# Performance work log

Hardware: AMD Instinct MI355X
Metric: run time of the kernel (lower is better)

Reference implementation:

```python
import jax, jax.numpy as jnp
import numpy as np
import math

B, S, H, NH = 4, 1024, 1024, 16
DH = H // NH
G = 100  # native graph size


def setup_inputs() -> dict:
    key = jax.random.key(0)
    ks = jax.random.split(key, 12)
    sc = 1.0 / math.sqrt(H)
    return {
        "v": jax.random.normal(ks[0], (B, S, H), jnp.float32),
        "k": jax.random.normal(ks[1], (B, S, H), jnp.float32),
        "q": jax.random.normal(ks[2], (B, S, H), jnp.float32),
        "mask": jax.random.randint(ks[3], (B, 1, 1, S), 0, 2) == 1,
        "graph": jax.random.uniform(ks[4], (B, G, G), jnp.float32),
        "Wq": jax.random.normal(ks[5], (H, H), jnp.float32) * sc,
        "bq": jnp.zeros((H,), jnp.float32),
        "Wk": jax.random.normal(ks[6], (H, H), jnp.float32) * sc,
        "bk": jnp.zeros((H,), jnp.float32),
        "Wv": jax.random.normal(ks[7], (H, H), jnp.float32) * sc,
        "bv": jnp.zeros((H,), jnp.float32),
        "Wm": jax.random.normal(ks[8], (H, H), jnp.float32) * sc,
        "bm": jnp.zeros((H,), jnp.float32),
    }


def _heads(x, W, b):
    # [B,S,H] -> [B,NH,S,DH]
    y = x @ W + b
    return y.reshape(B, S, NH, DH).transpose(0, 2, 1, 3)


def reference(v, k, q, mask, graph, Wq, bq, Wk, bk, Wv, bv, Wm, bm):
    qh = _heads(q, Wq, bq)
    kh = _heads(k, Wk, bk)
    vh = _heads(v, Wv, bv)
    scores = jnp.einsum("bhqd,bhkd->bhqk", qh, kh) / math.sqrt(DH)
    # pad 100x100 graph to SxS (zeros outside top-left block), as in torch source
    if S > G:
        graph = jnp.zeros((B, S, S), graph.dtype).at[:, :G, :G].set(graph)
    # scores - scores*graph, then mask fill and softmax
    scores = scores - scores * graph[:, None, :, :]
    scores = jnp.where(mask, jnp.float32(-1e9), scores)
    att = jax.nn.softmax(scores, axis=-1)  # dropout is identity in eval
    out = jnp.einsum("bhqk,bhkd->bhqd", att, vh)
    out = out.transpose(0, 2, 1, 3).reshape(B, S, H)
    return out @ Wm + bm
```

## Files before the change

kernel.cpp:

```cpp
#include <hip/hip_runtime.h>
#include <hip/hip_bf16.h>
#include <cstdio>

#define S_ 1024
#define H_ 1024
#define NH_ 16
#define DH_ 64
#define G_ 100

typedef __attribute__((ext_vector_type(8))) short bf16x8;
typedef __attribute__((ext_vector_type(4))) short bf16x4;
typedef __attribute__((ext_vector_type(4))) float f32x4;

__device__ __forceinline__ f32x4 mfma16(bf16x8 a, bf16x8 b, f32x4 c) {
  return __builtin_amdgcn_mfma_f32_16x16x32_bf16(a, b, c, 0, 0, 0);
}

__device__ __forceinline__ short f2bf(float f) {
  union { float f; unsigned int i; } x;
  x.f = f;
  unsigned int r = x.i + 0x7fff + ((x.i >> 16) & 1);
  return (short)(r >> 16);
}

__device__ __forceinline__ unsigned cvtpk(float lo, float hi) {
  unsigned r;
  asm("v_cvt_pk_bf16_f32 %0, %1, %2" : "=v"(r) : "v"(lo), "v"(hi));
  return r;
}

__device__ __forceinline__ float exp2hw(float x) {
  float r;
  asm("v_exp_f32 %0, %1" : "=v"(r) : "v"(x));
  return r;
}

__device__ __forceinline__ void gload16(const void* g, void* l) {
  __builtin_amdgcn_global_load_lds(
      (const __attribute__((address_space(1))) unsigned int*)g,
      (__attribute__((address_space(3))) unsigned int*)l, 16, 0, 0);
}

__global__ __launch_bounds__(256) void transpose_w(
    const float* __restrict__ W0, const float* __restrict__ W1,
    const float* __restrict__ W2, const float* __restrict__ W3,
    short* __restrict__ T0, short* __restrict__ T1,
    short* __restrict__ T2, short* __restrict__ T3) {
  __shared__ short tile[64][72];
  const float* W = (blockIdx.z == 0) ? W0 : (blockIdx.z == 1) ? W1
                 : (blockIdx.z == 2) ? W2 : W3;
  short* T = (blockIdx.z == 0) ? T0 : (blockIdx.z == 1) ? T1
           : (blockIdx.z == 2) ? T2 : T3;
  const int t = threadIdx.x;
  const int r0 = t >> 3;
  const int c8 = (t & 7) * 8;
  const int kbase = blockIdx.x * 64, nbase = blockIdx.y * 64;
#pragma unroll
  for (int p = 0; p < 2; ++p) {
    int r = p * 32 + r0;
    const float* src = W + (size_t)(kbase + r) * H_ + nbase + c8;
    f32x4 u0 = *reinterpret_cast<const f32x4*>(src);
    f32x4 u1 = *reinterpret_cast<const f32x4*>(src + 4);
#pragma unroll
    for (int j = 0; j < 4; ++j) {
      tile[r][c8 + j] = f2bf(u0[j]);
      tile[r][c8 + 4 + j] = f2bf(u1[j]);
    }
  }
  __syncthreads();
#pragma unroll
  for (int p = 0; p < 2; ++p) {
    int r = p * 32 + r0;
    bf16x8 o;
#pragma unroll
    for (int j = 0; j < 8; ++j) o[j] = tile[c8 + j][r];
    *reinterpret_cast<bf16x8*>(T + (size_t)(nbase + r) * H_ + kbase + c8) = o;
  }
}

__global__ __launch_bounds__(256, 3) void qkv128f(
    const float* __restrict__ A0, const float* __restrict__ A1,
    const float* __restrict__ A2, const short* __restrict__ W0,
    const short* __restrict__ W1, const short* __restrict__ W2,
    const float* __restrict__ b0, const float* __restrict__ b1,
    const float* __restrict__ b2, short* __restrict__ O0,
    short* __restrict__ O1, short* __restrict__ O2) {
  __shared__ float Af[2][128 * 32];
  __shared__ short Bs[2][128 * 32];
  const int z = blockIdx.z;
  const float* A  = (z == 0) ? A0 : (z == 1) ? A1 : A2;
  const short* Bt = (z == 0) ? W0 : (z == 1) ? W1 : W2;
  const float* bias = (z == 0) ? b0 : (z == 1) ? b1 : b2;
  short* Cb = (z == 0) ? O0 : (z == 1) ? O1 : O2;
  const float scale = (z == 0) ? 0.18033688f : 1.0f;
  const int K = H_;
  const int t = threadIdx.x;
  const int l = t & 63, w = t >> 6;
  const int lr = l & 15, lg = l >> 4;
  const int lx = lr & 7;
  const int lk = (lr >> 1) & 3;
  const int wm = w >> 1, wn = w & 1;
  const int bm = blockIdx.x * 128, bn = blockIdx.y * 128;
  f32x4 acc[4][4];
#pragma unroll
  for (int i = 0; i < 4; ++i)
#pragma unroll
    for (int j = 0; j < 4; ++j) acc[i][j] = (f32x4){0.f, 0.f, 0.f, 0.f};

  const int ar = t >> 3;
  const float* Ab = A + (size_t)(bm + ar) * K + ((t & 7) ^ (ar & 7)) * 4;
  const int br = t >> 2;
  const short* Bb =
      Bt + (size_t)(bn + br) * K + ((t & 3) ^ ((br >> 1) & 3)) * 8;

  auto stage = [&](int buf, int kb) {
#pragma unroll
    for (int p = 0; p < 4; ++p)
      gload16(Ab + (size_t)p * 32 * K + kb,
              (char*)&Af[buf][0] + p * 4096 + t * 16);
#pragma unroll
    for (int p = 0; p < 2; ++p)
      gload16(Bb + (size_t)p * 64 * K + kb,
              (char*)&Bs[buf][0] + p * 4096 + t * 16);
  };

  stage(0, 0);
  __syncthreads();
  const int NT = K >> 5;
  for (int tt = 0; tt < NT; ++tt) {
    const int cur = tt & 1;
    bf16x8 af[4], bfr[4];
#pragma unroll
    for (int mi = 0; mi < 4; ++mi) {
      const int row = wm * 64 + mi * 16 + lr;
      const float* Ar = &Af[cur][row * 32];
      f32x4 alo = *reinterpret_cast<const f32x4*>(Ar + (((lg * 2) ^ lx) * 4));
      f32x4 ahi =
          *reinterpret_cast<const f32x4*>(Ar + (((lg * 2 + 1) ^ lx) * 4));
      union { unsigned u[4]; bf16x8 v; } c;
      c.u[0] = cvtpk(alo[0], alo[1]);
      c.u[1] = cvtpk(alo[2], alo[3]);
      c.u[2] = cvtpk(ahi[0], ahi[1]);
      c.u[3] = cvtpk(ahi[2], ahi[3]);
      af[mi] = c.v;
    }
#pragma unroll
    for (int ni = 0; ni < 4; ++ni) {
      const int rb = wn * 64 + ni * 16 + lr;
      bfr[ni] = *reinterpret_cast<const bf16x8*>(
          &Bs[cur][rb * 32 + ((lg ^ lk) * 8)]);
    }
    if (tt + 1 < NT) stage(cur ^ 1, (tt + 1) << 5);
#pragma unroll
    for (int mi = 0; mi < 4; ++mi)
#pragma unroll
      for (int ni = 0; ni < 4; ++ni)
        acc[mi][ni] = mfma16(af[mi], bfr[ni], acc[mi][ni]);
    __syncthreads();
  }
#pragma unroll
  for (int mi = 0; mi < 4; ++mi)
#pragma unroll
    for (int ni = 0; ni < 4; ++ni) {
      int col = bn + wn * 64 + ni * 16 + lr;
      float bv = bias[col];
      int h = col >> 6, d = col & 63;
      if (z == 2) {
        int row0 = bm + wm * 64 + mi * 16 + lg * 4;
        int b = row0 >> 10, s0 = row0 & 1023;
        bf16x4 pk;
#pragma unroll
        for (int r = 0; r < 4; ++r) pk[r] = f2bf(acc[mi][ni][r] + bv);
        *reinterpret_cast<bf16x4*>(
            Cb + (((size_t)(b * NH_ + h)) * DH_ + d) * S_ + s0) = pk;
      } else {
#pragma unroll
        for (int r = 0; r < 4; ++r) {
          int row = bm + wm * 64 + mi * 16 + lg * 4 + r;
          int b = row >> 10, s = row & 1023;
          Cb[(((size_t)(b * NH_ + h)) * S_ + s) * DH_ + d] =
              f2bf((acc[mi][ni][r] + bv) * scale);
        }
      }
    }
}

__global__ __launch_bounds__(256) void out64(
    const short* __restrict__ A, const short* __restrict__ Bt,
    const float* __restrict__ bias, float* __restrict__ Cf) {
  __shared__ short As[2][64 * 32];
  __shared__ short Bs[2][128 * 32];
  const int K = H_, N = H_;
  const int t = threadIdx.x;
  const int l = t & 63, w = t >> 6;
  const int lr = l & 15, lg = l >> 4;
  const int lk = (lr >> 1) & 3;
  const int wm = w >> 1, wn = w & 1;
  const int bm = blockIdx.x * 64, bn = blockIdx.y * 128;
  f32x4 acc[2][4];
#pragma unroll
  for (int i = 0; i < 2; ++i)
#pragma unroll
    for (int j = 0; j < 4; ++j) acc[i][j] = (f32x4){0.f, 0.f, 0.f, 0.f};
  const int sr = t >> 2;
  const int ss = ((t & 3) ^ ((sr >> 1) & 3)) * 8;
  const short* Ab = A + (size_t)(bm + sr) * K + ss;
  const short* Bb = Bt + (size_t)(bn + sr) * K + ss;

  auto stage = [&](int buf, int kb) {
    gload16(Ab + kb, (char*)&As[buf][0] + t * 16);
    gload16(Bb + kb, (char*)&Bs[buf][0] + t * 16);
    gload16(Bb + (size_t)64 * K + kb, (char*)&Bs[buf][0] + 4096 + t * 16);
  };

  stage(0, 0);
  __syncthreads();
  const int NT = K >> 5;
  for (int tt = 0; tt < NT; ++tt) {
    const int cur = tt & 1;
    bf16x8 af[2], bfr[4];
#pragma unroll
    for (int mi = 0; mi < 2; ++mi) {
      const int row = wm * 32 + mi * 16 + lr;
      af[mi] = *reinterpret_cast<const bf16x8*>(
          &As[cur][row * 32 + ((lg ^ lk) * 8)]);
    }
#pragma unroll
    for (int ni = 0; ni < 4; ++ni) {
      const int rb = wn * 64 + ni * 16 + lr;
      bfr[ni] = *reinterpret_cast<const bf16x8*>(
          &Bs[cur][rb * 32 + ((lg ^ lk) * 8)]);
    }
    if (tt + 1 < NT) stage(cur ^ 1, (tt + 1) << 5);
#pragma unroll
    for (int mi = 0; mi < 2; ++mi)
#pragma unroll
      for (int ni = 0; ni < 4; ++ni)
        acc[mi][ni] = mfma16(af[mi], bfr[ni], acc[mi][ni]);
    __syncthreads();
  }
#pragma unroll
  for (int mi = 0; mi < 2; ++mi)
#pragma unroll
    for (int ni = 0; ni < 4; ++ni) {
      int col = bn + wn * 64 + ni * 16 + lr;
      float bv = bias[col];
#pragma unroll
      for (int r = 0; r < 4; ++r) {
        int row = bm + wm * 32 + mi * 16 + lg * 4 + r;
        Cf[(size_t)row * N + col] = acc[mi][ni][r] + bv;
      }
    }
}

__global__ __launch_bounds__(256) void attn(
    const short* __restrict__ Qh, const short* __restrict__ Kh,
    const short* __restrict__ VhT, const float* __restrict__ graph,
    const int* __restrict__ mask, short* __restrict__ ctx) {
  __shared__ short Kb[64 * 64];
  __shared__ short Vb[64 * 64];
  __shared__ short P[4 * 16 * 64];
  __shared__ float maskf[S_];
  const int lin = blockIdx.x;
  const int gid = (lin & 7) * 128 + (lin >> 3);
  const int bh = gid >> 4, qt = gid & 15;
  const int b = bh >> 4, h = bh & 15;
  const int t = threadIdx.x, w = t >> 6, l = t & 63;
  const int lr = l & 15, lg = l >> 4;
  const int lx = lr & 7;
  const int q0 = qt * 64 + w * 16;
  const int qg = q0 + lr;
  short* Pw = P + w * 1024;
  const short* Qrow = Qh + ((size_t)bh * S_ + qg) * DH_;
  bf16x8 qf0 = *reinterpret_cast<const bf16x8*>(Qrow + lg * 8);
  bf16x8 qf1 = *reinterpret_cast<const bf16x8*>(Qrow + 32 + lg * 8);
  f32x4 o[4];
#pragma unroll
  for (int i = 0; i < 4; ++i) o[i] = (f32x4){0.f, 0.f, 0.f, 0.f};
  float llp = 0.f;

  const int rs = t >> 2;
  const int ga = (t & 3) + ((rs & 1) << 2);
  const int gb = ga ^ 4;
  const int sw0 = ((ga ^ (rs & 7)) * 8);
  const int sw1 = ((gb ^ (rs & 7)) * 8);
  const short* Ksrc0 = Kh + ((size_t)bh * S_ + rs) * DH_ + ga * 8;
  const short* Ksrc1 = Kh + ((size_t)bh * S_ + rs) * DH_ + gb * 8;
  const short* Vsrc0 = VhT + ((size_t)bh * DH_ + rs) * S_ + ga * 8;
  const short* Vsrc1 = VhT + ((size_t)bh * DH_ + rs) * S_ + gb * 8;

  {
    int4 mv = reinterpret_cast<const int4*>(mask + b * S_)[t];
    f32x4 mo;
    const float C = -16.0f;
    mo.x = mv.x ? -1.0e9f : C;
    mo.y = mv.y ? -1.0e9f : C;
    mo.z = mv.z ? -1.0e9f : C;
    mo.w = mv.w ? -1.0e9f : C;
    reinterpret_cast<f32x4*>(maskf)[t] = mo;
  }
  {
    int4 ka = *reinterpret_cast<const int4*>(Ksrc0);
    int4 kb2 = *reinterpret_cast<const int4*>(Ksrc1);
    int4 va = *reinterpret_cast<const int4*>(Vsrc0);
    int4 vb2 = *reinterpret_cast<const int4*>(Vsrc1);
    *reinterpret_cast<int4*>(&Kb[rs * 64 + sw0]) = ka;
    *reinterpret_cast<int4*>(&Kb[rs * 64 + sw1]) = kb2;
    *reinterpret_cast<int4*>(&Vb[rs * 64 + sw0]) = va;
    *reinterpret_cast<int4*>(&Vb[rs * 64 + sw1]) = vb2;
  }
  __syncthreads();

  for (int kc = 0; kc < S_; kc += 64) {
    const bool pf = (kc + 64 < S_);
    int4 ka, kb2, va, vb2;
    if (pf) {
      ka = *reinterpret_cast<const int4*>(Ksrc0 + (size_t)(kc + 64) * DH_);
      kb2 = *reinterpret_cast<const int4*>(Ksrc1 + (size_t)(kc + 64) * DH_);
      va = *reinterpret_cast<const int4*>(Vsrc0 + kc + 64);
      vb2 = *reinterpret_cast<const int4*>(Vsrc1 + kc + 64);
    }
    f32x4 sacc[4];
    __builtin_amdgcn_s_setprio(1);
#pragma unroll
    for (int mf = 0; mf < 4; ++mf) {
      const int rk = mf * 16 + lr;
      bf16x8 k0 = *reinterpret_cast<const bf16x8*>(
          &Kb[rk * 64 + ((lg ^ lx) * 8)]);
      bf16x8 k1 = *reinterpret_cast<const bf16x8*>(
          &Kb[rk * 64 + (((4 + lg) ^ lx) * 8)]);
      f32x4 sa = (f32x4){0.f, 0.f, 0.f, 0.f};
      sa = mfma16(k0, qf0, sa);
      sa = mfma16(k1, qf1, sa);
      sacc[mf] = sa;
    }
    __builtin_amdgcn_s_setprio(0);
    const bool gblk = (q0 < G_) && (kc < G_);
    const int pw0 = lr * 64 + (lg & 1) * 4;
#pragma unroll
    for (int mf = 0; mf < 4; ++mf) {
      f32x4 mk = *reinterpret_cast<const f32x4*>(&maskf[kc + mf * 16 + lg * 4]);
      f32x4 sa = sacc[mf];
      if (gblk) {
#pragma unroll
        for (int r = 0; r < 4; ++r) {
          int kg = kc + mf * 16 + lg * 4 + r;
          if (qg < G_ && kg < G_)
            sa[r] *= (1.f - graph[((size_t)b * G_ + qg) * G_ + kg]);
        }
      }
      float e0 = exp2hw(sa[0] + mk[0]);
      float e1 = exp2hw(sa[1] + mk[1]);
      float e2 = exp2hw(sa[2] + mk[2]);
      float e3 = exp2hw(sa[3] + mk[3]);
      llp += (e0 + e1) + (e2 + e3);
      int2 pk2;
      pk2.x = (int)cvtpk(e0, e1);
      pk2.y = (int)cvtpk(e2, e3);
      *reinterpret_cast<int2*>(
          &Pw[pw0 + (((2 * mf + (lg >> 1)) ^ lx) * 8)]) = pk2;
    }
    __builtin_amdgcn_s_setprio(1);
#pragma unroll
    for (int ks = 0; ks < 2; ++ks) {
      bf16x8 pa = *reinterpret_cast<const bf16x8*>(
          &Pw[lr * 64 + (((ks * 4 + lg) ^ lx) * 8)]);
#pragma unroll
      for (int nf = 0; nf < 4; ++nf) {
        const int rv = nf * 16 + lr;
        bf16x8 vfr = *reinterpret_cast<const bf16x8*>(
            &Vb[rv * 64 + (((ks * 4 + lg) ^ lx) * 8)]);
        o[nf] = mfma16(pa, vfr, o[nf]);
      }
    }
    __builtin_amdgcn_s_setprio(0);
    if (pf) {
      __syncthreads();
      *reinterpret_cast<int4*>(&Kb[rs * 64 + sw0]) = ka;
      *reinterpret_cast<int4*>(&Kb[rs * 64 + sw1]) = kb2;
      *reinterpret_cast<int4*>(&Vb[rs * 64 + sw0]) = va;
      *reinterpret_cast<int4*>(&Vb[rs * 64 + sw1]) = vb2;
      __syncthreads();
    }
  }
  llp += __shfl_xor(llp, 16);
  llp += __shfl_xor(llp, 32);
  float rinv[4];
#pragma unroll
  for (int r = 0; r < 4; ++r)
    rinv[r] = __builtin_amdgcn_rcpf(__shfl(llp, lg * 4 + r, 64));
#pragma unroll
  for (int nf = 0; nf < 4; ++nf)
#pragma unroll
    for (int r = 0; r < 4; ++r) {
      float val = o[nf][r] * rinv[r];
      ctx[((size_t)b * S_ + q0 + lg * 4 + r) * H_ + h * DH_ + nf * 16 + lr] =
          f2bf(val);
    }
}

extern "C" void kernel_launch(void* const* d_in, const int* in_sizes, int n_in,
                              void* d_out, int out_size, void* d_ws, size_t ws_size,
                              hipStream_t stream) {
  const int B = in_sizes[0] / (S_ * H_);
  const int M = B * S_;
  const float* v    = (const float*)d_in[0];
  const float* k    = (const float*)d_in[1];
  const float* q    = (const float*)d_in[2];
  const int*   mask = (const int*)d_in[3];
  const float* graph= (const float*)d_in[4];
  const float* Wq   = (const float*)d_in[5];
  const float* bq   = (const float*)d_in[6];
  const float* Wk   = (const float*)d_in[7];
  const float* bk   = (const float*)d_in[8];
  const float* Wv   = (const float*)d_in[9];
  const float* bv   = (const float*)d_in[10];
  const float* Wm   = (const float*)d_in[11];
  const float* bm   = (const float*)d_in[12];

  short* ws = (short*)d_ws;
  const size_t WSZ = (size_t)H_ * H_;
  const size_t TSZ = (size_t)M * H_;
  short* WqT = ws;
  short* WkT = ws + WSZ;
  short* WvT = ws + 2 * WSZ;
  short* WmT = ws + 3 * WSZ;
  short* Qh  = ws + 4 * WSZ;
  short* Kh  = Qh + TSZ;
  short* VhT = Kh + TSZ;
  short* ctx = VhT + TSZ;
  if (ws_size < (4 * WSZ + 4 * TSZ) * sizeof(short)) {
    fprintf(stderr, "kernel_launch: ws too small (%zu)\n", ws_size);
    return;
  }

  transpose_w<<<dim3(H_ / 64, H_ / 64, 4), 256, 0, stream>>>(
      Wq, Wk, Wv, Wm, WqT, WkT, WvT, WmT);
  qkv128f<<<dim3(M / 128, H_ / 128, 3), 256, 0, stream>>>(
      q, k, v, WqT, WkT, WvT, bq, bk, bv, Qh, Kh, VhT);
  attn<<<dim3(1024), 256, 0, stream>>>(Qh, Kh, VhT, graph, mask, ctx);
  out64<<<dim3(M / 64, H_ / 128), 256, 0, stream>>>(
      ctx, WmT, bm, (float*)d_out);
}
```

Measured before the change: 106.9 us.

## Compact unmasked key positions and skip masked keys in K/V projection and attention

Adds a per-batch compaction kernel that builds a prefix-sum index list of unmasked key positions and their counts. The K and V projections then compute only rows for gathered unmasked positions, and attention iterates only over the compacted key range, with the graph term remapped through the index list. This is meant to cut projection and attention work roughly in proportion to the masked fraction. The cost is an extra small launch and gathered row loads. Padded tail rows in the last tile are filled with index 0 and hidden by the mask.

New measurement: 101.3 us, median of 2. -5.2%, faster.

```diff
diff --git a/kernel.cpp b/kernel.cpp
--- a/kernel.cpp
+++ b/kernel.cpp
@@ -39,6 +39,47 @@
   __builtin_amdgcn_global_load_lds(
       (const __attribute__((address_space(1))) unsigned int*)g,
       (__attribute__((address_space(3))) unsigned int*)l, 16, 0, 0);
+}
+
+__global__ __launch_bounds__(256) void compact(
+    const int* __restrict__ mask, int* __restrict__ idx,
+    int* __restrict__ cnts) {
+  __shared__ int ps[256];
+  __shared__ int scnt;
+  const int b = blockIdx.x, t = threadIdx.x;
+  int4 mv = reinterpret_cast<const int4*>(mask + b * S_)[t];
+  const int k0 = (mv.x == 0), k1 = (mv.y == 0), k2 = (mv.z == 0),
+            k3 = (mv.w == 0);
+  const int c = k0 + k1 + k2 + k3;
+  ps[t] = c;
+  __syncthreads();
+  for (int off = 1; off < 256; off <<= 1) {
+    int v = (t >= off) ? ps[t - off] : 0;
+    __syncthreads();
+    ps[t] += v;
+    __syncthreads();
+  }
+  int j = ps[t] - c;
+  const int s0 = t * 4;
+  if (k0) idx[b * S_ + j++] = s0;
+  if (k1) idx[b * S_ + j++] = s0 + 1;
+  if (k2) idx[b * S_ + j++] = s0 + 2;
+  if (k3) idx[b * S_ + j++] = s0 + 3;
+  if (t == 255) {
+    scnt = ps[255];
+    cnts[b] = ps[255];
+  }
+  __syncthreads();
+  for (int j2 = scnt + t; j2 < S_; j2 += 256) idx[b * S_ + j2] = 0;
+  int c100 = (k0 && s0 < G_) + (k1 && s0 + 1 < G_) + (k2 && s0 + 2 < G_) +
+             (k3 && s0 + 3 < G_);
+  ps[t] = c100;
+  __syncthreads();
+  for (int off = 128; off > 0; off >>= 1) {
+    if (t < off) ps[t] += ps[t + off];
+    __syncthreads();
+  }
+  if (t == 0) cnts[4 + b] = ps[0];
 }
 
 __global__ __launch_bounds__(256) void transpose_w(
@@ -84,7 +125,8 @@
     const short* __restrict__ W1, const short* __restrict__ W2,
     const float* __restrict__ b0, const float* __restrict__ b1,
     const float* __restrict__ b2, short* __restrict__ O0,
-    short* __restrict__ O1, short* __restrict__ O2) {
+    short* __restrict__ O1, short* __restrict__ O2,
+    const int* __restrict__ idx, const int* __restrict__ cnts) {
   __shared__ float Af[2][128 * 32];
   __shared__ short Bs[2][128 * 32];
   const int z = blockIdx.z;
@@ -101,62 +143,75 @@
   const int lk = (lr >> 1) & 3;
   const int wm = w >> 1, wn = w & 1;
   const int bm = blockIdx.x * 128, bn = blockIdx.y * 128;
+  const int bidx = bm >> 10;
+  const int jrow = bm & 1023;
+  const int cnt = (z == 0) ? 1024 : cnts[bidx];
   f32x4 acc[4][4];
 #pragma unroll
   for (int i = 0; i < 4; ++i)
 #pragma unroll
     for (int j = 0; j < 4; ++j) acc[i][j] = (f32x4){0.f, 0.f, 0.f, 0.f};
 
-  const int ar = t >> 3;
-  const float* Ab = A + (size_t)(bm + ar) * K + ((t & 7) ^ (ar & 7)) * 4;
-  const int br = t >> 2;
-  const short* Bb =
-      Bt + (size_t)(bn + br) * K + ((t & 3) ^ ((br >> 1) & 3)) * 8;
-
-  auto stage = [&](int buf, int kb) {
-#pragma unroll
-    for (int p = 0; p < 4; ++p)
-      gload16(Ab + (size_t)p * 32 * K + kb,
-              (char*)&Af[buf][0] + p * 4096 + t * 16);
-#pragma unroll
-    for (int p = 0; p < 2; ++p)
-      gload16(Bb + (size_t)p * 64 * K + kb,
-              (char*)&Bs[buf][0] + p * 4096 + t * 16);
-  };
-
-  stage(0, 0);
-  __syncthreads();
-  const int NT = K >> 5;
-  for (int tt = 0; tt < NT; ++tt) {
-    const int cur = tt & 1;
-    bf16x8 af[4], bfr[4];
-#pragma unroll
-    for (int mi = 0; mi < 4; ++mi) {
-      const int row = wm * 64 + mi * 16 + lr;
-      const float* Ar = &Af[cur][row * 32];
-      f32x4 alo = *reinterpret_cast<const f32x4*>(Ar + (((lg * 2) ^ lx) * 4));
-      f32x4 ahi =
-          *reinterpret_cast<const f32x4*>(Ar + (((lg * 2 + 1) ^ lx) * 4));
-      union { unsigned u[4]; bf16x8 v; } c;
-      c.u[0] = cvtpk(alo[0], alo[1]);
-      c.u[1] = cvtpk(alo[2], alo[3]);
-      c.u[2] = cvtpk(ahi[0], ahi[1]);
-      c.u[3] = cvtpk(ahi[2], ahi[3]);
-      af[mi] = c.v;
-    }
-#pragma unroll
-    for (int ni = 0; ni < 4; ++ni) {
-      const int rb = wn * 64 + ni * 16 + lr;
-      bfr[ni] = *reinterpret_cast<const bf16x8*>(
-          &Bs[cur][rb * 32 + ((lg ^ lk) * 8)]);
-    }
-    if (tt + 1 < NT) stage(cur ^ 1, (tt + 1) << 5);
-#pragma unroll
-    for (int mi = 0; mi < 4; ++mi)
-#pragma unroll
-      for (int ni = 0; ni < 4; ++ni)
-        acc[mi][ni] = mfma16(af[mi], bfr[ni], acc[mi][ni]);
+  if (jrow < cnt) {
+    const int ar = t >> 3;
+    const int acol = ((t & 7) ^ (ar & 7)) * 4;
+    const int* idxb = idx + bidx * 1024;
+    const float* Abp[4];
+#pragma unroll
+    for (int p = 0; p < 4; ++p) {
+      const int j = jrow + ar + p * 32;
+      const int srow = (z == 0) ? j : idxb[j];
+      Abp[p] = A + ((size_t)(bidx << 10) + srow) * K + acol;
+    }
+    const int br = t >> 2;
+    const short* Bb =
+        Bt + (size_t)(bn + br) * K + ((t & 3) ^ ((br >> 1) & 3)) * 8;
+
+    auto stage = [&](int buf, int kb) {
+#pragma unroll
+      for (int p = 0; p < 4; ++p)
+        gload16(Abp[p] + kb, (char*)&Af[buf][0] + p * 4096 + t * 16);
+#pragma unroll
+      for (int p = 0; p < 2; ++p)
+        gload16(Bb + (size_t)p * 64 * K + kb,
+                (char*)&Bs[buf][0] + p * 4096 + t * 16);
+    };
+
+    stage(0, 0);
     __syncthreads();
+    const int NT = K >> 5;
+    for (int tt = 0; tt < NT; ++tt) {
+      const int cur = tt & 1;
+      bf16x8 af[4], bfr[4];
+#pragma unroll
+      for (int mi = 0; mi < 4; ++mi) {
+        const int row = wm * 64 + mi * 16 + lr;
+        const float* Ar = &Af[cur][row * 32];
+        f32x4 alo =
+            *reinterpret_cast<const f32x4*>(Ar + (((lg * 2) ^ lx) * 4));
+        f32x4 ahi =
+            *reinterpret_cast<const f32x4*>(Ar + (((lg * 2 + 1) ^ lx) * 4));
+        union { unsigned u[4]; bf16x8 v; } c;
+        c.u[0] = cvtpk(alo[0], alo[1]);
+        c.u[1] = cvtpk(alo[2], alo[3]);
+        c.u[2] = cvtpk(ahi[0], ahi[1]);
+        c.u[3] = cvtpk(ahi[2], ahi[3]);
+        af[mi] = c.v;
+      }
+#pragma unroll
+      for (int ni = 0; ni < 4; ++ni) {
+        const int rb = wn * 64 + ni * 16 + lr;
+        bfr[ni] = *reinterpret_cast<const bf16x8*>(
+            &Bs[cur][rb * 32 + ((lg ^ lk) * 8)]);
+      }
+      if (tt + 1 < NT) stage(cur ^ 1, (tt + 1) << 5);
+#pragma unroll
+      for (int mi = 0; mi < 4; ++mi)
+#pragma unroll
+        for (int ni = 0; ni < 4; ++ni)
+          acc[mi][ni] = mfma16(af[mi], bfr[ni], acc[mi][ni]);
+      __syncthreads();
+    }
   }
 #pragma unroll
   for (int mi = 0; mi < 4; ++mi)
@@ -256,7 +311,8 @@
 __global__ __launch_bounds__(256) void attn(
     const short* __restrict__ Qh, const short* __restrict__ Kh,
     const short* __restrict__ VhT, const float* __restrict__ graph,
-    const int* __restrict__ mask, short* __restrict__ ctx) {
+    const int* __restrict__ idx, const int* __restrict__ cnts,
+    short* __restrict__ ctx) {
   __shared__ short Kb[64 * 64];
   __shared__ short Vb[64 * 64];
   __shared__ short P[4 * 16 * 64];
@@ -271,6 +327,10 @@
   const int q0 = qt * 64 + w * 16;
   const int qg = q0 + lr;
   short* Pw = P + w * 1024;
+  const int cnt = cnts[b];
+  const int cnt100 = cnts[4 + b];
+  const int kend = ((cnt + 63) >> 6) << 6;
+  const int* idxb = idx + b * 1024;
   const short* Qrow = Qh + ((size_t)bh * S_ + qg) * DH_;
   bf16x8 qf0 = *reinterpret_cast<const bf16x8*>(Qrow + lg * 8);
   bf16x8 qf1 = *reinterpret_cast<const bf16x8*>(Qrow + 32 + lg * 8);
@@ -290,13 +350,12 @@
   const short* Vsrc1 = VhT + ((size_t)bh * DH_ + rs) * S_ + gb * 8;
 
   {
-    int4 mv = reinterpret_cast<const int4*>(mask + b * S_)[t];
+    const int s0 = t * 4;
     f32x4 mo;
-    const float C = -16.0f;
-    mo.x = mv.x ? -1.0e9f : C;
-    mo.y = mv.y ? -1.0e9f : C;
-    mo.z = mv.z ? -1.0e9f : C;
-    mo.w = mv.w ? -1.0e9f : C;
+    mo.x = (s0 < cnt) ? -16.f : -1.0e9f;
+    mo.y = (s0 + 1 < cnt) ? -16.f : -1.0e9f;
+    mo.z = (s0 + 2 < cnt) ? -16.f : -1.0e9f;
+    mo.w = (s0 + 3 < cnt) ? -16.f : -1.0e9f;
     reinterpret_cast<f32x4*>(maskf)[t] = mo;
   }
   {
@@ -311,8 +370,8 @@
   }
   __syncthreads();
 
-  for (int kc = 0; kc < S_; kc += 64) {
-    const bool pf = (kc + 64 < S_);
+  for (int kc = 0; kc < kend; kc += 64) {
+    const bool pf = (kc + 64 < kend);
     int4 ka, kb2, va, vb2;
     if (pf) {
       ka = *reinterpret_cast<const int4*>(Ksrc0 + (size_t)(kc + 64) * DH_);
@@ -335,7 +394,7 @@
       sacc[mf] = sa;
     }
     __builtin_amdgcn_s_setprio(0);
-    const bool gblk = (q0 < G_) && (kc < G_);
+    const bool gblk = (q0 < G_) && (kc < cnt100);
     const int pw0 = lr * 64 + (lg & 1) * 4;
 #pragma unroll
     for (int mf = 0; mf < 4; ++mf) {
@@ -344,9 +403,9 @@
       if (gblk) {
 #pragma unroll
         for (int r = 0; r < 4; ++r) {
-          int kg = kc + mf * 16 + lg * 4 + r;
-          if (qg < G_ && kg < G_)
-            sa[r] *= (1.f - graph[((size_t)b * G_ + qg) * G_ + kg]);
+          int kgc = kc + mf * 16 + lg * 4 + r;
+          if (qg < G_ && kgc < cnt100)
+            sa[r] *= (1.f - graph[((size_t)b * G_ + qg) * G_ + idxb[kgc]]);
         }
       }
       float e0 = exp2hw(sa[0] + mk[0]);
@@ -429,16 +488,19 @@
   short* Kh  = Qh + TSZ;
   short* VhT = Kh + TSZ;
   short* ctx = VhT + TSZ;
-  if (ws_size < (4 * WSZ + 4 * TSZ) * sizeof(short)) {
+  int*   idxw = (int*)(ctx + TSZ);
+  int*   cntw = idxw + 4 * 1024;
+  if (ws_size < (4 * WSZ + 4 * TSZ) * sizeof(short) + (4 * 1024 + 8) * 4) {
     fprintf(stderr, "kernel_launch: ws too small (%zu)\n", ws_size);
     return;
   }
 
+  compact<<<dim3(4), 256, 0, stream>>>(mask, idxw, cntw);
   transpose_w<<<dim3(H_ / 64, H_ / 64, 4), 256, 0, stream>>>(
       Wq, Wk, Wv, Wm, WqT, WkT, WvT, WmT);
   qkv128f<<<dim3(M / 128, H_ / 128, 3), 256, 0, stream>>>(
-      q, k, v, WqT, WkT, WvT, bq, bk, bv, Qh, Kh, VhT);
-  attn<<<dim3(1024), 256, 0, stream>>>(Qh, Kh, VhT, graph, mask, ctx);
+      q, k, v, WqT, WkT, WvT, bq, bk, bv, Qh, Kh, VhT, idxw, cntw);
+  attn<<<dim3(1024), 256, 0, stream>>>(Qh, Kh, VhT, graph, idxw, cntw, ctx);
   out64<<<dim3(M / 64, H_ / 128), 256, 0, stream>>>(
       ctx, WmT, bm, (float*)d_out);
 }
```
